# Performance work log

Hardware: AMD Instinct MI355X
Metric: run time of the kernel (lower is better)

## Reference

```python
import jax, jax.numpy as jnp
import numpy as np

D = 2048; H = 16; DH = D // H; FF = 8192; PFF = 1024
EPS = 1e-6; THETA = 10000.0; CAPACITY = 0.5
BETA_CE = 1.0; BETA_CU = 1.0
SCALE = 0.02

def rms(x, w):
    return x * jax.lax.rsqrt(jnp.mean(x * x, axis=-1, keepdims=True) + EPS) * w

def rope(x, pos):
    # x: [B,H,T,DH], pos: [T]
    inv = 1.0 / (THETA ** (jnp.arange(0, DH, 2, dtype=jnp.float32) / DH))
    ang = pos[:, None] * inv[None, :]                      # [T, DH/2]
    cos = jnp.concatenate([jnp.cos(ang)] * 2, -1)          # [T, DH]
    sin = jnp.concatenate([jnp.sin(ang)] * 2, -1)
    x1, x2 = jnp.split(x, 2, axis=-1)
    rot = jnp.concatenate([-x2, x1], -1)
    return x * cos + rot * sin

def attention(x, wq, wk, wv, wo):
    B, T, _ = x.shape
    pos = jnp.arange(T, dtype=jnp.float32)
    q = (x @ wq).reshape(B, T, H, DH).transpose(0, 2, 1, 3)
    k = (x @ wk).reshape(B, T, H, DH).transpose(0, 2, 1, 3)
    v = (x @ wv).reshape(B, T, H, DH).transpose(0, 2, 1, 3)
    q = rope(q, pos); k = rope(k, pos)
    scores = jnp.einsum('bhqd,bhkd->bhqk', q, k) / np.sqrt(DH).astype(np.float32)
    mask = jnp.tril(jnp.ones((T, T), dtype=bool))
    scores = jnp.where(mask, scores, jnp.finfo(scores.dtype).min)
    probs = jax.nn.softmax(scores, axis=-1)
    out = jnp.einsum('bhqk,bhkd->bhqd', probs, v)
    return out.transpose(0, 2, 1, 3).reshape(B, T, D) @ wo

def swiglu(x, wg, wu, wd):
    return (jax.nn.silu(x @ wg) * (x @ wu)) @ wd

def decoder_layer(x, ln1, ln2, wq, wk, wv, wo, wg, wu, wd):
    h = x + attention(rms(x, ln1), wq, wk, wv, wo)
    return h + swiglu(rms(h, ln2), wg, wu, wd)

def setup_inputs() -> dict:
    key = jax.random.key(0)
    ks = iter(jax.random.split(key, 32))
    def w(shape):
        return SCALE * jax.random.normal(next(ks), shape, dtype=jnp.float32)
    inp = {'hidden_states': jax.random.normal(next(ks), (2, 2048, D), dtype=jnp.float32)}
    for p in ('d1', 'd2'):
        inp[p + '_ln1'] = jnp.ones((D,), jnp.float32)
        inp[p + '_ln2'] = jnp.ones((D,), jnp.float32)
        inp[p + '_wq'] = w((D, D)); inp[p + '_wk'] = w((D, D))
        inp[p + '_wv'] = w((D, D)); inp[p + '_wo'] = w((D, D))
        inp[p + '_wg'] = w((D, FF)); inp[p + '_wu'] = w((D, FF)); inp[p + '_wd'] = w((FF, D))
    inp['p_ln'] = jnp.ones((D,), jnp.float32)
    inp['p_wg'] = w((D, PFF)); inp['p_wu'] = w((D, PFF)); inp['p_wd'] = w((PFF, D))
    return inp

def reference(hidden_states,
              d1_ln1, d1_ln2, d1_wq, d1_wk, d1_wv, d1_wo, d1_wg, d1_wu, d1_wd,
              d2_ln1, d2_ln2, d2_wq, d2_wk, d2_wv, d2_wo, d2_wg, d2_wu, d2_wd,
              p_ln, p_wg, p_wu, p_wd):
    x = hidden_states
    B, T, _ = x.shape
    # decision layer: full decoder block + prior network
    processed = decoder_layer(x, d1_ln1, d1_ln2, d1_wq, d1_wk, d1_wv, d1_wo, d1_wg, d1_wu, d1_wd)
    prior_out = swiglu(rms(x, p_ln), p_wg, p_wu, p_wd)
    prior_hidden = x + prior_out
    actual_res = processed - x                 # [B,T,D]
    pred_res = prior_out                       # prior_hidden - x
    prior_loss = jnp.mean((prior_hidden - jax.lax.stop_gradient(processed)) ** 2)
    # surprise router (VPR-style gate)
    D_st = jnp.mean(actual_res ** 2, axis=-1)                    # [B,T]
    D_ch = jnp.mean((actual_res - pred_res) ** 2, axis=-1)       # [B,T]
    g_cont = jax.nn.sigmoid(BETA_CU * D_ch - BETA_CE * D_st)     # [B,T]
    # top-k token selection per batch row
    k = max(1, int(T * CAPACITY))
    gating_scores, topk_idx = jax.lax.top_k(g_cont, k)           # [B,k]
    # gather -> process through dynamic block -> soft-gate -> scatter
    sel = jnp.take_along_axis(processed, topk_idx[..., None], axis=1)   # [B,k,D]
    sel_out = decoder_layer(sel, d2_ln1, d2_ln2, d2_wq, d2_wk, d2_wv, d2_wo, d2_wg, d2_wu, d2_wd)
    updated = sel + gating_scores[..., None] * (sel_out - sel)   # soft gating (training)
    batch_idx = jnp.arange(B)[:, None]
    final = processed.at[batch_idx, topk_idx].set(updated)
    return final, prior_loss, g_cont
```

## Files before the change

kernel.cpp:

```cpp
#include <hip/hip_runtime.h>
#include <math.h>

#define D_    2048
#define H_    16
#define DH_   128
#define FF_   8192
#define PFF_  1024
#define B_    2
#define T_    2048
#define NTOK_ 4096
#define T2_   1024
#define NSEL_ 2048
#define EPS_  1e-6f
#define SCALE_QK 0.08838834764831845f

typedef __attribute__((ext_vector_type(8))) short bf16x8;
typedef __attribute__((ext_vector_type(4))) float f32x4;
typedef __attribute__((ext_vector_type(8))) unsigned short ushort8;

__device__ __forceinline__ float silu_f(float x) {
    return x / (1.0f + expf(-x));
}

__device__ __forceinline__ unsigned short bf16_rne(float f) {
    unsigned int u = __float_as_uint(f);
    unsigned int r = (u + 0x7fffu + ((u >> 16) & 1u)) >> 16;
    return (unsigned short)r;
}
__device__ __forceinline__ float bf16_tof(unsigned short h) {
    return __uint_as_float(((unsigned int)h) << 16);
}

__global__ __launch_bounds__(256) void rms_kernel(const float* __restrict__ x,
                                                  const float* __restrict__ w,
                                                  float* __restrict__ out) {
    int row = blockIdx.x;
    int tid = threadIdx.x;
    const float4* xr = (const float4*)(x + (size_t)row * D_);
    float4* orow = (float4*)(out + (size_t)row * D_);
    const float4* w4 = (const float4*)w;
    float4 v0 = xr[tid], v1 = xr[tid + 256];
    float s = v0.x*v0.x + v0.y*v0.y + v0.z*v0.z + v0.w*v0.w
            + v1.x*v1.x + v1.y*v1.y + v1.z*v1.z + v1.w*v1.w;
    __shared__ float red[256];
    red[tid] = s; __syncthreads();
    for (int off = 128; off > 0; off >>= 1) {
        if (tid < off) red[tid] += red[tid + off];
        __syncthreads();
    }
    float r = 1.0f / sqrtf(red[0] * (1.0f/2048.0f) + EPS_);
    float4 w0 = w4[tid], w1 = w4[tid + 256];
    float4 o0, o1;
    o0.x = v0.x*r*w0.x; o0.y = v0.y*r*w0.y; o0.z = v0.z*r*w0.z; o0.w = v0.w*r*w0.w;
    o1.x = v1.x*r*w1.x; o1.y = v1.y*r*w1.y; o1.z = v1.z*r*w1.z; o1.w = v1.w*r*w1.w;
    orow[tid] = o0; orow[tid + 256] = o1;
}

__global__ __launch_bounds__(256) void splitw_kernel(const float* __restrict__ W,
                                                     unsigned short* __restrict__ phi,
                                                     unsigned short* __restrict__ plo,
                                                     int K, int N) {
    __shared__ float Ts[64][68];
    int n0 = blockIdx.x << 6, k0 = blockIdx.y << 6;
    int tid = threadIdx.x;
#pragma unroll
    for (int it = 0; it < 4; ++it) {
        int idx = tid + (it << 8);
        int kr = idx >> 4, c4 = idx & 15;
        float4 v = *(const float4*)(W + (size_t)(k0 + kr) * N + n0 + (c4 << 2));
        Ts[kr][c4*4+0] = v.x; Ts[kr][c4*4+1] = v.y; Ts[kr][c4*4+2] = v.z; Ts[kr][c4*4+3] = v.w;
    }
    __syncthreads();
#pragma unroll
    for (int h = 0; h < 2; ++h) {
        int c = tid + (h << 8);
        int kc = c >> 6, n = c & 63;
        ushort8 hi, lo;
#pragma unroll
        for (int q = 0; q < 8; ++q) {
            float v = Ts[kc*8 + q][n];
            unsigned short hb = bf16_rne(v);
            hi[q] = hb;
            lo[q] = bf16_rne(v - bf16_tof(hb));
        }
        size_t off = ((size_t)((k0 >> 3) + kc) * N + (n0 + n)) * 8;
        *(ushort8*)(phi + off) = hi;
        *(ushort8*)(plo + off) = lo;
    }
}

__global__ __launch_bounds__(256) void splita_kernel(const float* __restrict__ A,
                                                     unsigned short* __restrict__ phi,
                                                     unsigned short* __restrict__ plo,
                                                     int M, int K) {
    __shared__ float Ts[64][68];
    int m0 = blockIdx.x << 6, k0 = blockIdx.y << 6;
    int tid = threadIdx.x;
#pragma unroll
    for (int it = 0; it < 4; ++it) {
        int idx = tid + (it << 8);
        int mr = idx >> 4, c4 = idx & 15;
        float4 v = *(const float4*)(A + (size_t)(m0 + mr) * K + k0 + (c4 << 2));
        Ts[mr][c4*4+0] = v.x; Ts[mr][c4*4+1] = v.y; Ts[mr][c4*4+2] = v.z; Ts[mr][c4*4+3] = v.w;
    }
    __syncthreads();
#pragma unroll
    for (int h = 0; h < 2; ++h) {
        int c = tid + (h << 8);
        int kc = c >> 6, m = c & 63;
        const float* src = &Ts[m][kc << 3];
        ushort8 hi, lo;
#pragma unroll
        for (int q = 0; q < 8; ++q) {
            float v = src[q];
            unsigned short hb = bf16_rne(v);
            hi[q] = hb;
            lo[q] = bf16_rne(v - bf16_tof(hb));
        }
        size_t off = ((size_t)((k0 >> 3) + kc) * M + (m0 + m)) * 8;
        *(ushort8*)(phi + off) = hi;
        *(ushort8*)(plo + off) = lo;
    }
}

__device__ __forceinline__ void stage_panel(unsigned short* lds,
                                            const unsigned short* __restrict__ panel,
                                            int ktile, int R, int brow, int tid) {
#pragma unroll
    for (int h = 0; h < 2; ++h) {
        int c = tid + (h << 8);
        const unsigned short* g = panel + ((size_t)((ktile << 2) + (c >> 7)) * R + (brow + (c & 127))) * 8;
        __builtin_amdgcn_global_load_lds((const __attribute__((address_space(1))) void*)g,
                                         (__attribute__((address_space(3))) void*)(lds + (size_t)c * 8),
                                         16, 0, 0);
    }
}

template<int NP, int EPI>
__global__ __launch_bounds__(256) void gemm_mfma(const unsigned short* __restrict__ pah,
                                                 const unsigned short* __restrict__ pal,
                                                 const unsigned short* __restrict__ pbh,
                                                 const unsigned short* __restrict__ pbl,
                                                 float* __restrict__ C,
                                                 const float* __restrict__ Rg,
                                                 int M, int N, int K) {
    __shared__ __align__(16) unsigned short As[2][4][128][8];
    __shared__ __align__(16) unsigned short Bs[2][4][128][8];
    const int tid = threadIdx.x;
    int nwg = gridDim.x * gridDim.y;
    int wg = blockIdx.y * gridDim.x + blockIdx.x;
    if ((nwg & 7) == 0) {
        int cpx = nwg >> 3;
        wg = (wg & 7) * cpx + (wg >> 3);
    }
    const int bxs = wg % gridDim.x, bys = wg / gridDim.x;
    const int bm = bys << 7, bn = bxs << 7;
    const int lane = tid & 63, wave = tid >> 6;
    const int wm = (wave >> 1) << 6, wn = (wave & 1) << 6;
    const int fr = lane & 15, fk = lane >> 4;

    f32x4 acc[4][4];
#pragma unroll
    for (int i = 0; i < 4; ++i)
#pragma unroll
        for (int j = 0; j < 4; ++j) acc[i][j] = (f32x4)0.0f;

    const int nkt = K >> 5;
    for (int kt = 0; kt < nkt; ++kt) {
        stage_panel(&As[0][0][0][0], pah, kt, M, bm, tid);
        if (NP == 3) stage_panel(&As[1][0][0][0], pal, kt, M, bm, tid);
        stage_panel(&Bs[0][0][0][0], pbh, kt, N, bn, tid);
        if (NP == 3) stage_panel(&Bs[1][0][0][0], pbl, kt, N, bn, tid);
        __syncthreads();

        bf16x8 ah[4], bh[4], al[4], bl[4];
#pragma unroll
        for (int i = 0; i < 4; ++i) {
            ah[i] = *(const bf16x8*)&As[0][fk][wm + (i << 4) + fr][0];
            if (NP == 3) al[i] = *(const bf16x8*)&As[1][fk][wm + (i << 4) + fr][0];
        }
#pragma unroll
        for (int j = 0; j < 4; ++j) {
            bh[j] = *(const bf16x8*)&Bs[0][fk][wn + (j << 4) + fr][0];
            if (NP == 3) bl[j] = *(const bf16x8*)&Bs[1][fk][wn + (j << 4) + fr][0];
        }
#pragma unroll
        for (int i = 0; i < 4; ++i)
#pragma unroll
            for (int j = 0; j < 4; ++j) {
                acc[i][j] = __builtin_amdgcn_mfma_f32_16x16x32_bf16(ah[i], bh[j], acc[i][j], 0, 0, 0);
                if (NP == 3) {
                    acc[i][j] = __builtin_amdgcn_mfma_f32_16x16x32_bf16(ah[i], bl[j], acc[i][j], 0, 0, 0);
                    acc[i][j] = __builtin_amdgcn_mfma_f32_16x16x32_bf16(al[i], bh[j], acc[i][j], 0, 0, 0);
                }
            }
        __syncthreads();
    }

#pragma unroll
    for (int i = 0; i < 4; ++i) {
        int row0 = bm + wm + (i << 4) + (fk << 2);
#pragma unroll
        for (int j = 0; j < 4; ++j) {
            int col = bn + wn + (j << 4) + fr;
#pragma unroll
            for (int r = 0; r < 4; ++r) {
                size_t off = (size_t)(row0 + r) * N + col;
                float v = acc[i][j][r];
                if (EPI == 1) v += Rg[off];
                else if (EPI == 2) { float g = Rg[off]; v = silu_f(g) * v; }
                C[off] = v;
            }
        }
    }
}

__global__ __launch_bounds__(256) void rope_split_kernel(const float* __restrict__ X,
                                                         unsigned short* __restrict__ xh,
                                                         unsigned short* __restrict__ xl,
                                                         int seqmask, float scale) {
    int tok = blockIdx.x;
    int tid = threadIdx.x;
    int h = tid >> 4, d0 = (tid & 15) << 3;
    int pos = tok & seqmask;
    const float* src = X + (size_t)tok * D_ + h * DH_;
    bool lohalf = d0 < 64;
    float out[8];
#pragma unroll
    for (int q = 0; q < 8; ++q) {
        int d = d0 + q;
        int i = lohalf ? d : (d - 64);
        float e = (float)(2 * i) * (1.0f / 128.0f);
        float inv = 1.0f / powf(10000.0f, e);
        float ang = (float)pos * inv;
        float c = cosf(ang), s = sinf(ang);
        float x1 = src[i], x2 = src[i + 64];
        out[q] = lohalf ? (x1 * c - x2 * s) : (x2 * c + x1 * s);
    }
    ushort8 hi, lo;
#pragma unroll
    for (int q = 0; q < 8; ++q) {
        float v = out[q] * scale;
        unsigned short hb = bf16_rne(v);
        hi[q] = hb;
        lo[q] = bf16_rne(v - bf16_tof(hb));
    }
    size_t off = (size_t)tok * D_ + h * DH_ + d0;
    *(ushort8*)(xh + off) = hi;
    *(ushort8*)(xl + off) = lo;
}

__global__ __launch_bounds__(256) void vpack_kernel(const float* __restrict__ V,
                                                    unsigned short* __restrict__ vth,
                                                    unsigned short* __restrict__ vtl,
                                                    int T) {
    __shared__ float Ts[64][132];
    int kt = blockIdx.x, bh = blockIdx.y;
    int b = bh >> 4, h = bh & 15;
    int tid = threadIdx.x;
#pragma unroll
    for (int it = 0; it < 8; ++it) {
        int idx = tid + (it << 8);
        int r = idx >> 5, c4 = idx & 31;
        float4 v = *(const float4*)(V + ((size_t)(b * T + kt * 64 + r)) * D_ + h * DH_ + (c4 << 2));
        Ts[r][c4*4+0] = v.x; Ts[r][c4*4+1] = v.y; Ts[r][c4*4+2] = v.z; Ts[r][c4*4+3] = v.w;
    }
    __syncthreads();
    size_t obase = ((size_t)bh * (size_t)(T >> 3) + (size_t)kt * 8) * 1024;
#pragma unroll
    for (int it = 0; it < 4; ++it) {
        int c = tid + (it << 8);
        int kc = c >> 7, dh = c & 127;
        ushort8 hi, lo;
#pragma unroll
        for (int q = 0; q < 8; ++q) {
            float v = Ts[kc * 8 + q][dh];
            unsigned short hb = bf16_rne(v);
            hi[q] = hb;
            lo[q] = bf16_rne(v - bf16_tof(hb));
        }
        *(ushort8*)(vth + obase + (size_t)kc * 1024 + dh * 8) = hi;
        *(ushort8*)(vtl + obase + (size_t)kc * 1024 + dh * 8) = lo;
    }
}

__global__ __launch_bounds__(256) void attn_mfma(const unsigned short* __restrict__ QH,
                                                 const unsigned short* __restrict__ QL,
                                                 const unsigned short* __restrict__ KH,
                                                 const unsigned short* __restrict__ KL,
                                                 const unsigned short* __restrict__ VTH,
                                                 const unsigned short* __restrict__ VTL,
                                                 float* __restrict__ O, int T) {
    __shared__ __align__(16) unsigned short KV[16384];
    __shared__ __align__(16) float Ss[4096];
    __shared__ __align__(16) float mrow[64];
    __shared__ __align__(16) float lrow[64];
    __shared__ __align__(16) float crow[64];

    const int tid = threadIdx.x;
    const int qt = blockIdx.x, bh = blockIdx.y;
    const int b = bh >> 4, h = bh & 15;
    const int lane = tid & 63, w = tid >> 6;
    const int fr = lane & 15, fk = lane >> 4;
    const size_t tok0 = (size_t)b * T;

    char* lds_kv = (char*)&KV[0];
    char* lds_sp = (char*)&Ss[0];

    bf16x8 qfh[4], qfl[4];
    {
        const size_t qoff = (tok0 + (size_t)qt * 64 + w * 16 + fr) * D_ + h * DH_ + fk * 8;
#pragma unroll
        for (int ks = 0; ks < 4; ++ks) {
            qfh[ks] = *(const bf16x8*)(QH + qoff + ks * 32);
            qfl[ks] = *(const bf16x8*)(QL + qoff + ks * 32);
        }
    }
    if (tid < 64) { mrow[tid] = -1e30f; lrow[tid] = 0.f; }

    f32x4 acc[8];
#pragma unroll
    for (int nt = 0; nt < 8; ++nt) acc[nt] = (f32x4)0.f;

    const int srow = tid >> 2, sslot = tid & 3;
    const size_t vbase = (size_t)bh * (size_t)(T >> 3) * 1024;

    for (int kt = 0; kt <= qt; ++kt) {
        __syncthreads();
#pragma unroll
        for (int it = 0; it < 4; ++it) {
            int c = tid + (it << 8);
            int t = c >> 4;
            int sp = (c & 15) ^ (t & 7);
            size_t goff = (tok0 + (size_t)kt * 64 + t) * D_ + h * DH_ + sp * 8;
            __builtin_amdgcn_global_load_lds((const __attribute__((address_space(1))) void*)(KH + goff),
                (__attribute__((address_space(3))) void*)(lds_kv + c * 16), 16, 0, 0);
            __builtin_amdgcn_global_load_lds((const __attribute__((address_space(1))) void*)(KL + goff),
                (__attribute__((address_space(3))) void*)(lds_kv + 16384 + c * 16), 16, 0, 0);
        }
        __syncthreads();
        {
            f32x4 s[4];
#pragma unroll
            for (int nt = 0; nt < 4; ++nt) s[nt] = (f32x4)0.f;
#pragma unroll
            for (int ks = 0; ks < 4; ++ks) {
#pragma unroll
                for (int nt = 0; nt < 4; ++nt) {
                    int n = nt * 16 + fr;
                    int offk = (n * 256 + ks * 64 + fk * 16) ^ ((n & 7) << 4);
                    bf16x8 kfh = *(const bf16x8*)(lds_kv + offk);
                    bf16x8 kfl = *(const bf16x8*)(lds_kv + 16384 + offk);
                    s[nt] = __builtin_amdgcn_mfma_f32_16x16x32_bf16(qfh[ks], kfh, s[nt], 0, 0, 0);
                    s[nt] = __builtin_amdgcn_mfma_f32_16x16x32_bf16(qfh[ks], kfl, s[nt], 0, 0, 0);
                    s[nt] = __builtin_amdgcn_mfma_f32_16x16x32_bf16(qfl[ks], kfh, s[nt], 0, 0, 0);
                }
            }
#pragma unroll
            for (int nt = 0; nt < 4; ++nt)
#pragma unroll
                for (int r = 0; r < 4; ++r) {
                    int row = w * 16 + fk * 4 + r;
                    int col = nt * 16 + fr;
                    *(float*)(lds_sp + ((row * 256 + col * 4) ^ ((row & 7) << 4))) = s[nt][r];
// ... 361 lines not shown
    }
}

__global__ __launch_bounds__(1024) void loss_kernel(const float* __restrict__ dch, float* __restrict__ out) {
    __shared__ float red[1024];
    int tid = threadIdx.x;
    red[tid] = dch[tid] + dch[tid + 1024] + dch[tid + 2048] + dch[tid + 3072];
    __syncthreads();
    for (int off = 512; off > 0; off >>= 1) {
        if (tid < off) red[tid] += red[tid + off];
        __syncthreads();
    }
    if (tid == 0) out[0] = red[0] * (1.0f / 4096.0f);
}

__global__ __launch_bounds__(1024) void topk_kernel(const float* __restrict__ gbuf,
                                                    int* __restrict__ idxout,
                                                    float* __restrict__ gateout) {
    int b = blockIdx.x, tid = threadIdx.x;
    __shared__ float val[2048];
    __shared__ int idx[2048];
    val[tid] = gbuf[b*2048 + tid];           idx[tid] = tid;
    val[tid + 1024] = gbuf[b*2048 + tid + 1024]; idx[tid + 1024] = tid + 1024;
    __syncthreads();
    for (int kk = 2; kk <= 2048; kk <<= 1) {
        for (int j = kk >> 1; j > 0; j >>= 1) {
            for (int i = tid; i < 2048; i += 1024) {
                int ixj = i ^ j;
                if (ixj > i) {
                    bool up = ((i & kk) == 0);
                    float v1 = val[i], v2 = val[ixj];
                    int i1 = idx[i], i2 = idx[ixj];
                    bool sw = up ? ((v2 > v1) || (v2 == v1 && i2 < i1))
                                 : ((v1 > v2) || (v1 == v2 && i1 < i2));
                    if (sw) { val[i] = v2; val[ixj] = v1; idx[i] = i2; idx[ixj] = i1; }
                }
            }
            __syncthreads();
        }
    }
    if (tid < 1024) {
        idxout[b*1024 + tid] = idx[tid];
        gateout[b*1024 + tid] = val[tid];
    }
}

__global__ __launch_bounds__(256) void gather_kernel(const float* __restrict__ proc,
                                                     const int* __restrict__ idx,
                                                     float* __restrict__ sel) {
    int r = blockIdx.x;
    int b = r >> 10, rr = r & 1023;
    int tok = idx[b*1024 + rr];
    const float4* src = (const float4*)(proc + ((size_t)(b*2048 + tok)) * D_);
    float4* dst = (float4*)(sel + (size_t)r * D_);
    dst[threadIdx.x] = src[threadIdx.x];
    dst[threadIdx.x + 256] = src[threadIdx.x + 256];
}

__global__ __launch_bounds__(256) void copy_kernel(const float* __restrict__ src,
                                                   float* __restrict__ dst, int n4) {
    int i = blockIdx.x * 256 + threadIdx.x;
    if (i < n4) ((float4*)dst)[i] = ((const float4*)src)[i];
}

__global__ __launch_bounds__(256) void scatter_kernel(const float* __restrict__ sel,
                                                      const float* __restrict__ selout,
                                                      const int* __restrict__ idx,
                                                      const float* __restrict__ gate,
                                                      float* __restrict__ outp) {
    int r = blockIdx.x;
    int b = r >> 10, rr = r & 1023;
    int tok = idx[b*1024 + rr];
    float g = gate[b*1024 + rr];
    const float4* s4 = (const float4*)(sel + (size_t)r * D_);
    const float4* o4 = (const float4*)(selout + (size_t)r * D_);
    float4* d4 = (float4*)(outp + ((size_t)(b*2048 + tok)) * D_);
#pragma unroll
    for (int it = 0; it < 2; ++it) {
        int i = threadIdx.x + it * 256;
        float4 a = s4[i], o = o4[i];
        float4 w;
        w.x = a.x + g*(o.x - a.x); w.y = a.y + g*(o.y - a.y);
        w.z = a.z + g*(o.z - a.z); w.w = a.w + g*(o.w - a.w);
        d4[i] = w;
    }
}

extern "C" void kernel_launch(void* const* d_in, const int* in_sizes, int n_in,
                              void* d_out, int out_size, void* d_ws, size_t ws_size,
                              hipStream_t stream) {
    const float* X      = (const float*)d_in[0];
    const float* d1_ln1 = (const float*)d_in[1];
    const float* d1_ln2 = (const float*)d_in[2];
    const float* d1_wq  = (const float*)d_in[3];
    const float* d1_wk  = (const float*)d_in[4];
    const float* d1_wv  = (const float*)d_in[5];
    const float* d1_wo  = (const float*)d_in[6];
    const float* d1_wg  = (const float*)d_in[7];
    const float* d1_wu  = (const float*)d_in[8];
    const float* d1_wd  = (const float*)d_in[9];
    const float* d2_ln1 = (const float*)d_in[10];
    const float* d2_ln2 = (const float*)d_in[11];
    const float* d2_wq  = (const float*)d_in[12];
    const float* d2_wk  = (const float*)d_in[13];
    const float* d2_wv  = (const float*)d_in[14];
    const float* d2_wo  = (const float*)d_in[15];
    const float* d2_wg  = (const float*)d_in[16];
    const float* d2_wu  = (const float*)d_in[17];
    const float* d2_wd  = (const float*)d_in[18];
    const float* p_ln   = (const float*)d_in[19];
    const float* p_wg   = (const float*)d_in[20];
    const float* p_wu   = (const float*)d_in[21];
    const float* p_wd   = (const float*)d_in[22];

    float* out = (float*)d_out;
    float* ws  = (float*)d_ws;

    const size_t BIG = (size_t)NTOK_ * D_;
    const size_t MEG = 1024 * 1024;

    const size_t NEED_NEW = (128 * MEG + 16384) * 4;
    const size_t NEED_OLD = ((5*BIG + (size_t)NTOK_*FF_ + 12288) * 4);

    if (ws_size >= NEED_NEW) {
        float* BUF0 = ws;
        float* BUF1 = ws + 8*MEG;
        float* BUF2 = ws + 16*MEG;
        float* BUF3 = ws + 24*MEG;
        float* BUF4 = ws + 32*MEG;
        float* BUFF = ws + 40*MEG;
        unsigned short* PWhi  = (unsigned short*)(ws + 72*MEG);
        unsigned short* PWlo  = (unsigned short*)(ws + 80*MEG);
        unsigned short* PAhi  = (unsigned short*)(ws + 88*MEG);
        unsigned short* PAlo  = (unsigned short*)(ws + 92*MEG);
        unsigned short* PFhi  = (unsigned short*)(ws + 96*MEG);
        unsigned short* PFlo  = (unsigned short*)(ws + 112*MEG);
        unsigned short* U   = (unsigned short*)(ws + 96*MEG);
        const size_t PK = (size_t)NTOK_ * D_;
        unsigned short* QHp = U;
        unsigned short* QLp = U + PK;
        unsigned short* KHp = U + 2*PK;
        unsigned short* KLp = U + 3*PK;
        unsigned short* VTH = U + 4*PK;
        unsigned short* VTL = U + 5*PK;
        float* SM   = ws + 128*MEG;
        float* gbuf = SM;
        float* dch  = SM + 4096;
        float* gate = SM + 8192;
        int*   idxb = (int*)(SM + 10240);

        rms_kernel<<<NTOK_, 256, 0, stream>>>(X, d1_ln1, BUF0);
        splita_kernel<<<dim3(64, 32), 256, 0, stream>>>(BUF0, PAhi, PAlo, NTOK_, D_);
        splitw_kernel<<<dim3(32, 32), 256, 0, stream>>>(d1_wq, PWhi, PWlo, D_, D_);
        gemm_mfma<3,0><<<dim3(16, 32), 256, 0, stream>>>(PAhi, PAlo, PWhi, PWlo, BUF1, nullptr, NTOK_, D_, D_);
        splitw_kernel<<<dim3(32, 32), 256, 0, stream>>>(d1_wk, PWhi, PWlo, D_, D_);
        gemm_mfma<3,0><<<dim3(16, 32), 256, 0, stream>>>(PAhi, PAlo, PWhi, PWlo, BUF2, nullptr, NTOK_, D_, D_);
        splitw_kernel<<<dim3(32, 32), 256, 0, stream>>>(d1_wv, PWhi, PWlo, D_, D_);
        gemm_mfma<3,0><<<dim3(16, 32), 256, 0, stream>>>(PAhi, PAlo, PWhi, PWlo, BUF3, nullptr, NTOK_, D_, D_);
        rope_split_kernel<<<NTOK_, 256, 0, stream>>>(BUF1, QHp, QLp, T_ - 1, SCALE_QK);
        rope_split_kernel<<<NTOK_, 256, 0, stream>>>(BUF2, KHp, KLp, T_ - 1, 1.0f);
        vpack_kernel<<<dim3(T_/64, B_*H_), 256, 0, stream>>>(BUF3, VTH, VTL, T_);
        attn_mfma<<<dim3(T_/64, B_*H_), 256, 0, stream>>>(QHp, QLp, KHp, KLp, VTH, VTL, BUF4, T_);
        splita_kernel<<<dim3(64, 32), 256, 0, stream>>>(BUF4, PAhi, PAlo, NTOK_, D_);
        splitw_kernel<<<dim3(32, 32), 256, 0, stream>>>(d1_wo, PWhi, PWlo, D_, D_);
        gemm_mfma<3,1><<<dim3(16, 32), 256, 0, stream>>>(PAhi, PAlo, PWhi, PWlo, BUF2, X, NTOK_, D_, D_);
        rms_kernel<<<NTOK_, 256, 0, stream>>>(BUF2, d1_ln2, BUF0);
        splita_kernel<<<dim3(64, 32), 256, 0, stream>>>(BUF0, PAhi, PAlo, NTOK_, D_);
        splitw_kernel<<<dim3(128, 32), 256, 0, stream>>>(d1_wg, PWhi, PWlo, D_, FF_);
        gemm_mfma<3,0><<<dim3(64, 32), 256, 0, stream>>>(PAhi, PAlo, PWhi, PWlo, BUFF, nullptr, NTOK_, FF_, D_);
        splitw_kernel<<<dim3(128, 32), 256, 0, stream>>>(d1_wu, PWhi, PWlo, D_, FF_);
        gemm_mfma<3,2><<<dim3(64, 32), 256, 0, stream>>>(PAhi, PAlo, PWhi, PWlo, BUFF, BUFF, NTOK_, FF_, D_);
        splita_kernel<<<dim3(64, 128), 256, 0, stream>>>(BUFF, PFhi, PFlo, NTOK_, FF_);
        splitw_kernel<<<dim3(32, 128), 256, 0, stream>>>(d1_wd, PWhi, PWlo, FF_, D_);
        gemm_mfma<3,1><<<dim3(16, 32), 256, 0, stream>>>(PFhi, PFlo, PWhi, PWlo, BUF1, BUF2, NTOK_, D_, FF_);

        rms_kernel<<<NTOK_, 256, 0, stream>>>(X, p_ln, BUF0);
        splita_kernel<<<dim3(64, 32), 256, 0, stream>>>(BUF0, PAhi, PAlo, NTOK_, D_);
        splitw_kernel<<<dim3(16, 32), 256, 0, stream>>>(p_wg, PWhi, PWlo, D_, PFF_);
        gemm_mfma<3,0><<<dim3(8, 32), 256, 0, stream>>>(PAhi, PAlo, PWhi, PWlo, BUFF, nullptr, NTOK_, PFF_, D_);
        splitw_kernel<<<dim3(16, 32), 256, 0, stream>>>(p_wu, PWhi, PWlo, D_, PFF_);
        gemm_mfma<3,2><<<dim3(8, 32), 256, 0, stream>>>(PAhi, PAlo, PWhi, PWlo, BUFF, BUFF, NTOK_, PFF_, D_);
        splita_kernel<<<dim3(64, 16), 256, 0, stream>>>(BUFF, PFhi, PFlo, NTOK_, PFF_);
        splitw_kernel<<<dim3(32, 16), 256, 0, stream>>>(p_wd, PWhi, PWlo, PFF_, D_);
        gemm_mfma<3,0><<<dim3(16, 32), 256, 0, stream>>>(PFhi, PFlo, PWhi, PWlo, BUF3, nullptr, NTOK_, D_, PFF_);

        router_kernel<<<NTOK_, 256, 0, stream>>>(X, BUF1, BUF3, gbuf, dch, out + 8388609);
        loss_kernel<<<1, 1024, 0, stream>>>(dch, out + 8388608);
        topk_kernel<<<B_, 1024, 0, stream>>>(gbuf, idxb, gate);
        gather_kernel<<<NSEL_, 256, 0, stream>>>(BUF1, idxb, BUF4);

        float* V2 = BUF4 + (size_t)NSEL_ * D_;
        rms_kernel<<<NSEL_, 256, 0, stream>>>(BUF4, d2_ln1, BUF0);
        splita_kernel<<<dim3(32, 32), 256, 0, stream>>>(BUF0, PAhi, PAlo, NSEL_, D_);
        splitw_kernel<<<dim3(32, 32), 256, 0, stream>>>(d2_wq, PWhi, PWlo, D_, D_);
        gemm_mfma<1,0><<<dim3(16, 16), 256, 0, stream>>>(PAhi, PAlo, PWhi, PWlo, BUF2, nullptr, NSEL_, D_, D_);
        splitw_kernel<<<dim3(32, 32), 256, 0, stream>>>(d2_wk, PWhi, PWlo, D_, D_);
        gemm_mfma<1,0><<<dim3(16, 16), 256, 0, stream>>>(PAhi, PAlo, PWhi, PWlo, BUF3, nullptr, NSEL_, D_, D_);
        splitw_kernel<<<dim3(32, 32), 256, 0, stream>>>(d2_wv, PWhi, PWlo, D_, D_);
        gemm_mfma<1,0><<<dim3(16, 16), 256, 0, stream>>>(PAhi, PAlo, PWhi, PWlo, V2, nullptr, NSEL_, D_, D_);
        rope_split_kernel<<<NSEL_, 256, 0, stream>>>(BUF2, QHp, QLp, T2_ - 1, SCALE_QK);
        rope_split_kernel<<<NSEL_, 256, 0, stream>>>(BUF3, KHp, KLp, T2_ - 1, 1.0f);
        vpack_kernel<<<dim3(T2_/64, B_*H_), 256, 0, stream>>>(V2, VTH, VTL, T2_);
        attn_mfma<<<dim3(T2_/64, B_*H_), 256, 0, stream>>>(QHp, QLp, KHp, KLp, VTH, VTL, BUF0, T2_);
        splita_kernel<<<dim3(32, 32), 256, 0, stream>>>(BUF0, PAhi, PAlo, NSEL_, D_);
        splitw_kernel<<<dim3(32, 32), 256, 0, stream>>>(d2_wo, PWhi, PWlo, D_, D_);
        gemm_mfma<1,1><<<dim3(16, 16), 256, 0, stream>>>(PAhi, PAlo, PWhi, PWlo, BUF2, BUF4, NSEL_, D_, D_);
        rms_kernel<<<NSEL_, 256, 0, stream>>>(BUF2, d2_ln2, BUF0);
        splita_kernel<<<dim3(32, 32), 256, 0, stream>>>(BUF0, PAhi, PAlo, NSEL_, D_);
        splitw_kernel<<<dim3(128, 32), 256, 0, stream>>>(d2_wg, PWhi, PWlo, D_, FF_);
        gemm_mfma<1,0><<<dim3(64, 16), 256, 0, stream>>>(PAhi, PAlo, PWhi, PWlo, BUFF, nullptr, NSEL_, FF_, D_);
        splitw_kernel<<<dim3(128, 32), 256, 0, stream>>>(d2_wu, PWhi, PWlo, D_, FF_);
        gemm_mfma<1,2><<<dim3(64, 16), 256, 0, stream>>>(PAhi, PAlo, PWhi, PWlo, BUFF, BUFF, NSEL_, FF_, D_);
        splita_kernel<<<dim3(32, 128), 256, 0, stream>>>(BUFF, PFhi, PFlo, NSEL_, FF_);
        splitw_kernel<<<dim3(32, 128), 256, 0, stream>>>(d2_wd, PWhi, PWlo, FF_, D_);
        gemm_mfma<1,1><<<dim3(16, 16), 256, 0, stream>>>(PFhi, PFlo, PWhi, PWlo, BUF3, BUF2, NSEL_, D_, FF_);

        copy_kernel<<<8192, 256, 0, stream>>>(BUF1, out, (int)(BIG / 4));
        scatter_kernel<<<NSEL_, 256, 0, stream>>>(BUF4, BUF3, idxb, gate, out);
        return;
    }

    if (ws_size < NEED_OLD) return;

    float* BUF0 = ws;
    float* BUF1 = ws + BIG;
    float* BUF2 = ws + 2*BIG;
    float* BUF3 = ws + 3*BIG;
    float* BUF4 = ws + 4*BIG;
    float* BUFF = ws + 5*BIG;
    float* SM   = BUFF + (size_t)NTOK_ * FF_;
    float* gbuf = SM;
    float* dch  = SM + 4096;
    float* gate = SM + 8192;
    int*   idxb = (int*)(SM + 10240);

    rms_kernel<<<NTOK_, 256, 0, stream>>>(X, d1_ln1, BUF0);
    gemm128<0><<<dim3(16, 32), 256, 0, stream>>>(BUF0, d1_wq, BUF1, nullptr, NTOK_, D_, D_);
    gemm128<0><<<dim3(16, 32), 256, 0, stream>>>(BUF0, d1_wk, BUF2, nullptr, NTOK_, D_, D_);
    gemm128<0><<<dim3(16, 32), 256, 0, stream>>>(BUF0, d1_wv, BUF3, nullptr, NTOK_, D_, D_);
    rope_kernel<<<NTOK_*4, 256, 0, stream>>>(BUF1, NTOK_, T_);
    rope_kernel<<<NTOK_*4, 256, 0, stream>>>(BUF2, NTOK_, T_);
    attn_kernel<<<dim3(T_/32, B_*H_), 256, 0, stream>>>(BUF1, BUF2, BUF3, BUF4, T_);
    gemm128<1><<<dim3(16, 32), 256, 0, stream>>>(BUF4, d1_wo, BUF2, X, NTOK_, D_, D_);
    rms_kernel<<<NTOK_, 256, 0, stream>>>(BUF2, d1_ln2, BUF0);
    gemm128<0><<<dim3(64, 32), 256, 0, stream>>>(BUF0, d1_wg, BUFF, nullptr, NTOK_, FF_, D_);
    gemm128<2><<<dim3(64, 32), 256, 0, stream>>>(BUF0, d1_wu, BUFF, BUFF, NTOK_, FF_, D_);
    gemm128<1><<<dim3(16, 32), 256, 0, stream>>>(BUFF, d1_wd, BUF1, BUF2, NTOK_, D_, FF_);

    rms_kernel<<<NTOK_, 256, 0, stream>>>(X, p_ln, BUF0);
    gemm128<0><<<dim3(8, 32), 256, 0, stream>>>(BUF0, p_wg, BUF4, nullptr, NTOK_, PFF_, D_);
    gemm128<2><<<dim3(8, 32), 256, 0, stream>>>(BUF0, p_wu, BUF4, BUF4, NTOK_, PFF_, D_);
    gemm128<0><<<dim3(16, 32), 256, 0, stream>>>(BUF4, p_wd, BUF3, nullptr, NTOK_, D_, PFF_);

    router_kernel<<<NTOK_, 256, 0, stream>>>(X, BUF1, BUF3, gbuf, dch, out + 8388609);
    loss_kernel<<<1, 1024, 0, stream>>>(dch, out + 8388608);
    topk_kernel<<<B_, 1024, 0, stream>>>(gbuf, idxb, gate);
    gather_kernel<<<NSEL_, 256, 0, stream>>>(BUF1, idxb, BUF4);

    float* V2 = BUF4 + (size_t)NSEL_ * D_;
    rms_kernel<<<NSEL_, 256, 0, stream>>>(BUF4, d2_ln1, BUF0);
    gemm128<0><<<dim3(16, 16), 256, 0, stream>>>(BUF0, d2_wq, BUF2, nullptr, NSEL_, D_, D_);
    gemm128<0><<<dim3(16, 16), 256, 0, stream>>>(BUF0, d2_wk, BUF3, nullptr, NSEL_, D_, D_);
    gemm128<0><<<dim3(16, 16), 256, 0, stream>>>(BUF0, d2_wv, V2, nullptr, NSEL_, D_, D_);
    rope_kernel<<<NSEL_*4, 256, 0, stream>>>(BUF2, NSEL_, T2_);
    rope_kernel<<<NSEL_*4, 256, 0, stream>>>(BUF3, NSEL_, T2_);
    attn_kernel<<<dim3(T2_/32, B_*H_), 256, 0, stream>>>(BUF2, BUF3, V2, BUF0, T2_);
    gemm128<1><<<dim3(16, 16), 256, 0, stream>>>(BUF0, d2_wo, BUF2, BUF4, NSEL_, D_, D_);
    rms_kernel<<<NSEL_, 256, 0, stream>>>(BUF2, d2_ln2, BUF0);
    gemm128<0><<<dim3(64, 16), 256, 0, stream>>>(BUF0, d2_wg, BUFF, nullptr, NSEL_, FF_, D_);
    gemm128<2><<<dim3(64, 16), 256, 0, stream>>>(BUF0, d2_wu, BUFF, BUFF, NSEL_, FF_, D_);
    gemm128<1><<<dim3(16, 16), 256, 0, stream>>>(BUFF, d2_wd, BUF3, BUF2, NSEL_, D_, FF_);

    copy_kernel<<<8192, 256, 0, stream>>>(BUF1, out, (int)(BIG / 4));
    scatter_kernel<<<NSEL_, 256, 0, stream>>>(BUF4, BUF3, idxb, gate, out);
}
```

Before: 3.472 ms.

## Double-buffer GEMM LDS staging and fuse SwiGLU output into bf16 panel split

The GEMM main loop now uses two LDS buffers and prefetches the next K tile while computing the current one, which removes one barrier per iteration and overlaps global-to-LDS loads with MFMA work. LDS use is sized by panel count, so the single-panel variant keeps a similar footprint. The SwiGLU up-projection epilogue now writes the silu-gated product directly as packed bf16 hi/lo panels (hi only for the single-panel path), which removes the separate fp32 write and the splita pass over the large FF intermediate. The cost is doubled LDS for the three-panel variant, which may lower occupancy, plus scattered 2-byte stores in the packed-panel epilogue.

```diff
diff --git a/kernel.cpp b/kernel.cpp
--- a/kernel.cpp
+++ b/kernel.cpp
@@ -143,9 +143,12 @@
                                                  const unsigned short* __restrict__ pbl,
                                                  float* __restrict__ C,
                                                  const float* __restrict__ Rg,
+                                                 unsigned short* __restrict__ Cph,
+                                                 unsigned short* __restrict__ Cpl,
                                                  int M, int N, int K) {
-    __shared__ __align__(16) unsigned short As[2][4][128][8];
-    __shared__ __align__(16) unsigned short Bs[2][4][128][8];
+    constexpr int NPAN = (NP == 3) ? 2 : 1;
+    __shared__ __align__(16) unsigned short As[2][NPAN][4][128][8];
+    __shared__ __align__(16) unsigned short Bs[2][NPAN][4][128][8];
     const int tid = threadIdx.x;
     int nwg = gridDim.x * gridDim.y;
     int wg = blockIdx.y * gridDim.x + blockIdx.x;
@@ -166,23 +169,33 @@
         for (int j = 0; j < 4; ++j) acc[i][j] = (f32x4)0.0f;
 
     const int nkt = K >> 5;
+
+    stage_panel(&As[0][0][0][0][0], pah, 0, M, bm, tid);
+    if (NP == 3) stage_panel(&As[0][1][0][0][0], pal, 0, M, bm, tid);
+    stage_panel(&Bs[0][0][0][0][0], pbh, 0, N, bn, tid);
+    if (NP == 3) stage_panel(&Bs[0][1][0][0][0], pbl, 0, N, bn, tid);
+    __syncthreads();
+
+    int cur = 0;
     for (int kt = 0; kt < nkt; ++kt) {
-        stage_panel(&As[0][0][0][0], pah, kt, M, bm, tid);
-        if (NP == 3) stage_panel(&As[1][0][0][0], pal, kt, M, bm, tid);
-        stage_panel(&Bs[0][0][0][0], pbh, kt, N, bn, tid);
-        if (NP == 3) stage_panel(&Bs[1][0][0][0], pbl, kt, N, bn, tid);
-        __syncthreads();
+        if (kt + 1 < nkt) {
+            int nxt = cur ^ 1;
+            stage_panel(&As[nxt][0][0][0][0], pah, kt + 1, M, bm, tid);
+            if (NP == 3) stage_panel(&As[nxt][1][0][0][0], pal, kt + 1, M, bm, tid);
+            stage_panel(&Bs[nxt][0][0][0][0], pbh, kt + 1, N, bn, tid);
+            if (NP == 3) stage_panel(&Bs[nxt][1][0][0][0], pbl, kt + 1, N, bn, tid);
+        }
 
         bf16x8 ah[4], bh[4], al[4], bl[4];
 #pragma unroll
         for (int i = 0; i < 4; ++i) {
-            ah[i] = *(const bf16x8*)&As[0][fk][wm + (i << 4) + fr][0];
-            if (NP == 3) al[i] = *(const bf16x8*)&As[1][fk][wm + (i << 4) + fr][0];
+            ah[i] = *(const bf16x8*)&As[cur][0][fk][wm + (i << 4) + fr][0];
+            if (NP == 3) al[i] = *(const bf16x8*)&As[cur][NPAN-1][fk][wm + (i << 4) + fr][0];
         }
 #pragma unroll
         for (int j = 0; j < 4; ++j) {
-            bh[j] = *(const bf16x8*)&Bs[0][fk][wn + (j << 4) + fr][0];
-            if (NP == 3) bl[j] = *(const bf16x8*)&Bs[1][fk][wn + (j << 4) + fr][0];
+            bh[j] = *(const bf16x8*)&Bs[cur][0][fk][wn + (j << 4) + fr][0];
+            if (NP == 3) bl[j] = *(const bf16x8*)&Bs[cur][NPAN-1][fk][wn + (j << 4) + fr][0];
         }
 #pragma unroll
         for (int i = 0; i < 4; ++i)
@@ -195,6 +208,7 @@
                 }
             }
         __syncthreads();
+        cur ^= 1;
     }
 
 #pragma unroll
@@ -205,11 +219,22 @@
             int col = bn + wn + (j << 4) + fr;
 #pragma unroll
             for (int r = 0; r < 4; ++r) {
-                size_t off = (size_t)(row0 + r) * N + col;
+                int row = row0 + r;
+                size_t off = (size_t)row * N + col;
                 float v = acc[i][j][r];
-                if (EPI == 1) v += Rg[off];
-                else if (EPI == 2) { float g = Rg[off]; v = silu_f(g) * v; }
-                C[off] = v;
+                if (EPI == 0) {
+                    C[off] = v;
+                } else if (EPI == 1) {
+                    C[off] = v + Rg[off];
+                } else if (EPI == 2) {
+                    C[off] = silu_f(Rg[off]) * v;
+                } else {
+                    v = silu_f(Rg[off]) * v;
+                    unsigned short hb = bf16_rne(v);
+                    size_t poff = (((size_t)(col >> 3)) * M + row) * 8 + (col & 7);
+                    Cph[poff] = hb;
+                    if (EPI == 3) Cpl[poff] = bf16_rne(v - bf16_tof(hb));
+                }
             }
         }
     }
@@ -877,37 +902,35 @@
         rms_kernel<<<NTOK_, 256, 0, stream>>>(X, d1_ln1, BUF0);
         splita_kernel<<<dim3(64, 32), 256, 0, stream>>>(BUF0, PAhi, PAlo, NTOK_, D_);
         splitw_kernel<<<dim3(32, 32), 256, 0, stream>>>(d1_wq, PWhi, PWlo, D_, D_);
-        gemm_mfma<3,0><<<dim3(16, 32), 256, 0, stream>>>(PAhi, PAlo, PWhi, PWlo, BUF1, nullptr, NTOK_, D_, D_);
+        gemm_mfma<3,0><<<dim3(16, 32), 256, 0, stream>>>(PAhi, PAlo, PWhi, PWlo, BUF1, nullptr, nullptr, nullptr, NTOK_, D_, D_);
         splitw_kernel<<<dim3(32, 32), 256, 0, stream>>>(d1_wk, PWhi, PWlo, D_, D_);
-        gemm_mfma<3,0><<<dim3(16, 32), 256, 0, stream>>>(PAhi, PAlo, PWhi, PWlo, BUF2, nullptr, NTOK_, D_, D_);
+        gemm_mfma<3,0><<<dim3(16, 32), 256, 0, stream>>>(PAhi, PAlo, PWhi, PWlo, BUF2, nullptr, nullptr, nullptr, NTOK_, D_, D_);
         splitw_kernel<<<dim3(32, 32), 256, 0, stream>>>(d1_wv, PWhi, PWlo, D_, D_);
-        gemm_mfma<3,0><<<dim3(16, 32), 256, 0, stream>>>(PAhi, PAlo, PWhi, PWlo, BUF3, nullptr, NTOK_, D_, D_);
+        gemm_mfma<3,0><<<dim3(16, 32), 256, 0, stream>>>(PAhi, PAlo, PWhi, PWlo, BUF3, nullptr, nullptr, nullptr, NTOK_, D_, D_);
         rope_split_kernel<<<NTOK_, 256, 0, stream>>>(BUF1, QHp, QLp, T_ - 1, SCALE_QK);
         rope_split_kernel<<<NTOK_, 256, 0, stream>>>(BUF2, KHp, KLp, T_ - 1, 1.0f);
         vpack_kernel<<<dim3(T_/64, B_*H_), 256, 0, stream>>>(BUF3, VTH, VTL, T_);
         attn_mfma<<<dim3(T_/64, B_*H_), 256, 0, stream>>>(QHp, QLp, KHp, KLp, VTH, VTL, BUF4, T_);
         splita_kernel<<<dim3(64, 32), 256, 0, stream>>>(BUF4, PAhi, PAlo, NTOK_, D_);
         splitw_kernel<<<dim3(32, 32), 256, 0, stream>>>(d1_wo, PWhi, PWlo, D_, D_);
-        gemm_mfma<3,1><<<dim3(16, 32), 256, 0, stream>>>(PAhi, PAlo, PWhi, PWlo, BUF2, X, NTOK_, D_, D_);
+        gemm_mfma<3,1><<<dim3(16, 32), 256, 0, stream>>>(PAhi, PAlo, PWhi, PWlo, BUF2, X, nullptr, nullptr, NTOK_, D_, D_);
         rms_kernel<<<NTOK_, 256, 0, stream>>>(BUF2, d1_ln2, BUF0);
         splita_kernel<<<dim3(64, 32), 256, 0, stream>>>(BUF0, PAhi, PAlo, NTOK_, D_);
         splitw_kernel<<<dim3(128, 32), 256, 0, stream>>>(d1_wg, PWhi, PWlo, D_, FF_);
-        gemm_mfma<3,0><<<dim3(64, 32), 256, 0, stream>>>(PAhi, PAlo, PWhi, PWlo, BUFF, nullptr, NTOK_, FF_, D_);
+        gemm_mfma<3,0><<<dim3(64, 32), 256, 0, stream>>>(PAhi, PAlo, PWhi, PWlo, BUFF, nullptr, nullptr, nullptr, NTOK_, FF_, D_);
         splitw_kernel<<<dim3(128, 32), 256, 0, stream>>>(d1_wu, PWhi, PWlo, D_, FF_);
-        gemm_mfma<3,2><<<dim3(64, 32), 256, 0, stream>>>(PAhi, PAlo, PWhi, PWlo, BUFF, BUFF, NTOK_, FF_, D_);
-        splita_kernel<<<dim3(64, 128), 256, 0, stream>>>(BUFF, PFhi, PFlo, NTOK_, FF_);
+        gemm_mfma<3,3><<<dim3(64, 32), 256, 0, stream>>>(PAhi, PAlo, PWhi, PWlo, nullptr, BUFF, PFhi, PFlo, NTOK_, FF_, D_);
         splitw_kernel<<<dim3(32, 128), 256, 0, stream>>>(d1_wd, PWhi, PWlo, FF_, D_);
-        gemm_mfma<3,1><<<dim3(16, 32), 256, 0, stream>>>(PFhi, PFlo, PWhi, PWlo, BUF1, BUF2, NTOK_, D_, FF_);
+        gemm_mfma<3,1><<<dim3(16, 32), 256, 0, stream>>>(PFhi, PFlo, PWhi, PWlo, BUF1, BUF2, nullptr, nullptr, NTOK_, D_, FF_);
 
         rms_kernel<<<NTOK_, 256, 0, stream>>>(X, p_ln, BUF0);
         splita_kernel<<<dim3(64, 32), 256, 0, stream>>>(BUF0, PAhi, PAlo, NTOK_, D_);
         splitw_kernel<<<dim3(16, 32), 256, 0, stream>>>(p_wg, PWhi, PWlo, D_, PFF_);
-        gemm_mfma<3,0><<<dim3(8, 32), 256, 0, stream>>>(PAhi, PAlo, PWhi, PWlo, BUFF, nullptr, NTOK_, PFF_, D_);
+        gemm_mfma<3,0><<<dim3(8, 32), 256, 0, stream>>>(PAhi, PAlo, PWhi, PWlo, BUFF, nullptr, nullptr, nullptr, NTOK_, PFF_, D_);
         splitw_kernel<<<dim3(16, 32), 256, 0, stream>>>(p_wu, PWhi, PWlo, D_, PFF_);
-        gemm_mfma<3,2><<<dim3(8, 32), 256, 0, stream>>>(PAhi, PAlo, PWhi, PWlo, BUFF, BUFF, NTOK_, PFF_, D_);
-        splita_kernel<<<dim3(64, 16), 256, 0, stream>>>(BUFF, PFhi, PFlo, NTOK_, PFF_);
+        gemm_mfma<3,3><<<dim3(8, 32), 256, 0, stream>>>(PAhi, PAlo, PWhi, PWlo, nullptr, BUFF, PFhi, PFlo, NTOK_, PFF_, D_);
         splitw_kernel<<<dim3(32, 16), 256, 0, stream>>>(p_wd, PWhi, PWlo, PFF_, D_);
-        gemm_mfma<3,0><<<dim3(16, 32), 256, 0, stream>>>(PFhi, PFlo, PWhi, PWlo, BUF3, nullptr, NTOK_, D_, PFF_);
+        gemm_mfma<3,0><<<dim3(16, 32), 256, 0, stream>>>(PFhi, PFlo, PWhi, PWlo, BUF3, nullptr, nullptr, nullptr, NTOK_, D_, PFF_);
 
         router_kernel<<<NTOK_, 256, 0, stream>>>(X, BUF1, BUF3, gbuf, dch, out + 8388609);
         loss_kernel<<<1, 1024, 0, stream>>>(dch, out + 8388608);
@@ -918,27 +941,26 @@
         rms_kernel<<<NSEL_, 256, 0, stream>>>(BUF4, d2_ln1, BUF0);
         splita_kernel<<<dim3(32, 32), 256, 0, stream>>>(BUF0, PAhi, PAlo, NSEL_, D_);
         splitw_kernel<<<dim3(32, 32), 256, 0, stream>>>(d2_wq, PWhi, PWlo, D_, D_);
-        gemm_mfma<1,0><<<dim3(16, 16), 256, 0, stream>>>(PAhi, PAlo, PWhi, PWlo, BUF2, nullptr, NSEL_, D_, D_);
+        gemm_mfma<1,0><<<dim3(16, 16), 256, 0, stream>>>(PAhi, PAlo, PWhi, PWlo, BUF2, nullptr, nullptr, nullptr, NSEL_, D_, D_);
         splitw_kernel<<<dim3(32, 32), 256, 0, stream>>>(d2_wk, PWhi, PWlo, D_, D_);
-        gemm_mfma<1,0><<<dim3(16, 16), 256, 0, stream>>>(PAhi, PAlo, PWhi, PWlo, BUF3, nullptr, NSEL_, D_, D_);
+        gemm_mfma<1,0><<<dim3(16, 16), 256, 0, stream>>>(PAhi, PAlo, PWhi, PWlo, BUF3, nullptr, nullptr, nullptr, NSEL_, D_, D_);
         splitw_kernel<<<dim3(32, 32), 256, 0, stream>>>(d2_wv, PWhi, PWlo, D_, D_);
-        gemm_mfma<1,0><<<dim3(16, 16), 256, 0, stream>>>(PAhi, PAlo, PWhi, PWlo, V2, nullptr, NSEL_, D_, D_);
+        gemm_mfma<1,0><<<dim3(16, 16), 256, 0, stream>>>(PAhi, PAlo, PWhi, PWlo, V2, nullptr, nullptr, nullptr, NSEL_, D_, D_);
         rope_split_kernel<<<NSEL_, 256, 0, stream>>>(BUF2, QHp, QLp, T2_ - 1, SCALE_QK);
         rope_split_kernel<<<NSEL_, 256, 0, stream>>>(BUF3, KHp, KLp, T2_ - 1, 1.0f);
         vpack_kernel<<<dim3(T2_/64, B_*H_), 256, 0, stream>>>(V2, VTH, VTL, T2_);
         attn_mfma<<<dim3(T2_/64, B_*H_), 256, 0, stream>>>(QHp, QLp, KHp, KLp, VTH, VTL, BUF0, T2_);
         splita_kernel<<<dim3(32, 32), 256, 0, stream>>>(BUF0, PAhi, PAlo, NSEL_, D_);
         splitw_kernel<<<dim3(32, 32), 256, 0, stream>>>(d2_wo, PWhi, PWlo, D_, D_);
-        gemm_mfma<1,1><<<dim3(16, 16), 256, 0, stream>>>(PAhi, PAlo, PWhi, PWlo, BUF2, BUF4, NSEL_, D_, D_);
+        gemm_mfma<1,1><<<dim3(16, 16), 256, 0, stream>>>(PAhi, PAlo, PWhi, PWlo, BUF2, BUF4, nullptr, nullptr, NSEL_, D_, D_);
         rms_kernel<<<NSEL_, 256, 0, stream>>>(BUF2, d2_ln2, BUF0);
         splita_kernel<<<dim3(32, 32), 256, 0, stream>>>(BUF0, PAhi, PAlo, NSEL_, D_);
         splitw_kernel<<<dim3(128, 32), 256, 0, stream>>>(d2_wg, PWhi, PWlo, D_, FF_);
-        gemm_mfma<1,0><<<dim3(64, 16), 256, 0, stream>>>(PAhi, PAlo, PWhi, PWlo, BUFF, nullptr, NSEL_, FF_, D_);
+        gemm_mfma<1,0><<<dim3(64, 16), 256, 0, stream>>>(PAhi, PAlo, PWhi, PWlo, BUFF, nullptr, nullptr, nullptr, NSEL_, FF_, D_);
         splitw_kernel<<<dim3(128, 32), 256, 0, stream>>>(d2_wu, PWhi, PWlo, D_, FF_);
-        gemm_mfma<1,2><<<dim3(64, 16), 256, 0, stream>>>(PAhi, PAlo, PWhi, PWlo, BUFF, BUFF, NSEL_, FF_, D_);
-        splita_kernel<<<dim3(32, 128), 256, 0, stream>>>(BUFF, PFhi, PFlo, NSEL_, FF_);
+        gemm_mfma<1,4><<<dim3(64, 16), 256, 0, stream>>>(PAhi, PAlo, PWhi, PWlo, nullptr, BUFF, PFhi, nullptr, NSEL_, FF_, D_);
         splitw_kernel<<<dim3(32, 128), 256, 0, stream>>>(d2_wd, PWhi, PWlo, FF_, D_);
-        gemm_mfma<1,1><<<dim3(16, 16), 256, 0, stream>>>(PFhi, PFlo, PWhi, PWlo, BUF3, BUF2, NSEL_, D_, FF_);
+        gemm_mfma<1,1><<<dim3(16, 16), 256, 0, stream>>>(PFhi, PFlo, PWhi, PWlo, BUF3, BUF2, nullptr, nullptr, NSEL_, D_, FF_);
 
         copy_kernel<<<8192, 256, 0, stream>>>(BUF1, out, (int)(BIG / 4));
         scatter_kernel<<<NSEL_, 256, 0, stream>>>(BUF4, BUF3, idxb, gate, out);
```

After: 3.214 ms. 1.08x faster.
